# Performance work log

Hardware: AMD Instinct MI355X
Metric: run time of the kernel (lower is better)

Reference implementation:

```python
import jax, jax.numpy as jnp
import numpy as np

EMBED = 1024
HEADS = 16
HEAD_DIM = EMBED // HEADS


def setup_inputs() -> dict:
    key = jax.random.key(0)
    ks = jax.random.split(key, 9)
    s = 1.0 / np.sqrt(EMBED)
    inp = {
        "inputs": jax.random.normal(ks[0], (2, 2048, EMBED), dtype=jnp.float32),
        "Wq": jax.random.normal(ks[1], (EMBED, EMBED), dtype=jnp.float32) * s,
        "bq": jnp.zeros((EMBED,), dtype=jnp.float32),
        "Wk": jax.random.normal(ks[2], (EMBED, EMBED), dtype=jnp.float32) * s,
        "bk": jnp.zeros((EMBED,), dtype=jnp.float32),
        "Wv": jax.random.normal(ks[3], (EMBED, EMBED), dtype=jnp.float32) * s,
        "bv": jnp.zeros((EMBED,), dtype=jnp.float32),
        "Wo": jax.random.normal(ks[4], (EMBED, EMBED), dtype=jnp.float32) * s,
        "bo": jnp.zeros((EMBED,), dtype=jnp.float32),
    }
    return inp


def _split_heads(x, B, S):
    # [B, S, E] -> [B, H, S, D]
    return x.reshape(B, S, HEADS, HEAD_DIM).transpose(0, 2, 1, 3)


def reference(inputs, Wq, bq, Wk, bk, Wv, bv, Wo, bo):
    B, S, E = inputs.shape
    q = _split_heads(inputs @ Wq + bq, B, S)
    k = _split_heads(inputs @ Wk + bk, B, S)
    v = _split_heads(inputs @ Wv + bv, B, S)
    # scaled dot-product attention per the original: score scaled by sqrt(d_k)
    score = jnp.einsum("bhsd,bhtd->bhst", q, k) / jnp.sqrt(jnp.float32(HEAD_DIM))
    weights = jax.nn.softmax(score, axis=-1)
    attn = jnp.einsum("bhst,bhtd->bhsd", weights, v)
    concat = attn.transpose(0, 2, 1, 3).reshape(B, S, E)
    return concat @ Wo + bo
```

## Files before the change

kernel.cpp:

```cpp
#include <hip/hip_runtime.h>
#include <cmath>

#define EMBED 1024
#define HEADS 16
#define HDIM  64
#define BATCH 2
#define SEQ   2048
#define MTOT  (BATCH*SEQ)
#define KDIM  1024

typedef __attribute__((ext_vector_type(8))) short bf16x8;
typedef __attribute__((ext_vector_type(4))) float fx4;

#define MFMA(a,b,c) __builtin_amdgcn_mfma_f32_16x16x32_bf16((a),(b),(c),0,0,0)

__device__ __forceinline__ unsigned short f2bf(float x) {
    unsigned u = __float_as_uint(x);
    unsigned r = (u + 0x7FFFu + ((u >> 16) & 1u)) >> 16;
    return (unsigned short)r;
}
__device__ __forceinline__ float bf2f(unsigned short h) {
    return __uint_as_float(((unsigned)h) << 16);
}
__device__ __forceinline__ int swz_grp(int row, int grp) {
    return row * 64 + ((grp ^ (row & 7)) << 3);
}
__device__ __forceinline__ void gload16(const void* g, void* l) {
    __builtin_amdgcn_global_load_lds((const __attribute__((address_space(1))) void*)g,
                                     (__attribute__((address_space(3))) void*)l, 16, 0, 0);
}
__device__ __forceinline__ float dpp_qswap(float x) {
    return __int_as_float(__builtin_amdgcn_mov_dpp(__float_as_int(x), 0xB1, 0xF, 0xF, true));
}

#define C2S 0.18033688f

__global__ __launch_bounds__(256)
void prep(const float* __restrict__ X,
          const float* __restrict__ Wq, const float* __restrict__ Wk,
          const float* __restrict__ Wv, const float* __restrict__ Wo,
          unsigned short* __restrict__ Xh,
          unsigned short* __restrict__ WtH, unsigned short* __restrict__ WtL,
          unsigned short* __restrict__ WtOh, unsigned short* __restrict__ WtOl)
{
    const int bid = blockIdx.x;
    const int tid = threadIdx.x;
    if (bid < 2048) {
        int i = (bid * 256 + tid) * 8;
        float4 a = *(const float4*)(X + i);
        float4 b = *(const float4*)(X + i + 4);
        bf16x8 h;
        h[0] = (short)f2bf(a.x); h[1] = (short)f2bf(a.y);
        h[2] = (short)f2bf(a.z); h[3] = (short)f2bf(a.w);
        h[4] = (short)f2bf(b.x); h[5] = (short)f2bf(b.y);
        h[6] = (short)f2bf(b.z); h[7] = (short)f2bf(b.w);
        *(bf16x8*)(Xh + i) = h;
        return;
    }
    const int u = bid - 2048;
    const int z = u >> 8;
    const float* W = (z == 0) ? Wq : (z == 1) ? Wk : (z == 2) ? Wv : Wo;
    unsigned short* Th = (z < 3) ? WtH + (size_t)z * 1048576 : WtOh;
    unsigned short* Tl = (z == 2) ? WtL + (size_t)2 * 1048576 : WtOl;
    const bool wantLo = (z >= 2);
    const int k0 = ((u >> 4) & 15) * 64, n0 = (u & 15) * 64;

    __shared__ float t[64][65];
    #pragma unroll
    for (int it = 0; it < 4; ++it) {
        int v2 = tid + it * 256;
        int r = v2 >> 4, c4 = (v2 & 15) << 2;
        float4 v = *(const float4*)(W + (size_t)(k0 + r) * EMBED + n0 + c4);
        t[r][c4] = v.x; t[r][c4 + 1] = v.y; t[r][c4 + 2] = v.z; t[r][c4 + 3] = v.w;
    }
    __syncthreads();
    #pragma unroll
    for (int it = 0; it < 4; ++it) {
        int v2 = tid + it * 256;
        int r = v2 >> 4, c4 = (v2 & 15) << 2;
        ushort4 h, l;
        float x;
        x = t[c4 + 0][r]; h.x = f2bf(x); l.x = f2bf(x - bf2f(h.x));
        x = t[c4 + 1][r]; h.y = f2bf(x); l.y = f2bf(x - bf2f(h.y));
        x = t[c4 + 2][r]; h.z = f2bf(x); l.z = f2bf(x - bf2f(h.z));
        x = t[c4 + 3][r]; h.w = f2bf(x); l.w = f2bf(x - bf2f(h.w));
        *(ushort4*)(Th + (size_t)(n0 + r) * EMBED + k0 + c4) = h;
        if (wantLo)
            *(ushort4*)(Tl + (size_t)(n0 + r) * EMBED + k0 + c4) = l;
    }
}

__global__ __launch_bounds__(256, 2)
void gemm_qkv(const unsigned short* __restrict__ Xh,
              const unsigned short* __restrict__ WtH, const unsigned short* __restrict__ WtL,
              const float* __restrict__ bq, const float* __restrict__ bk,
              const float* __restrict__ bv,
              unsigned short* __restrict__ Qh, unsigned short* __restrict__ Khi,
              unsigned short* __restrict__ Vhi)
{
    __shared__ unsigned short Ah[8192];
    __shared__ unsigned short Bh[3][4096], Bl[4096];

    const int tid = threadIdx.x, lane = tid & 63, w = tid >> 6;
    const int wm = w >> 1, wn = w & 1;
    const int lin = (blockIdx.x & 7) * 64 + (blockIdx.x >> 3);
    const int m0 = (lin >> 4) * 128, n0 = (lin & 15) * 64;

    const char* aB = (const char*)(Xh + (size_t)m0 * KDIM);

    auto stageA = [&](int kt) {
        #pragma unroll
        for (int i = 0; i < 4; ++i) {
            int uw = (i << 12) + (w << 10);
            int u  = uw + (lane << 4);
            int row = u >> 7, grp = (u >> 4) & 7;
            size_t gb = (size_t)row * (KDIM * 2) + (size_t)kt * 128 + ((grp ^ (row & 7)) << 4);
            gload16(aB + gb, (char*)Ah + uw);
        }
    };
    auto stageB = [&](int kt, int which) {
        const char* bBh = (const char*)(WtH + (size_t)which * 1048576 + (size_t)n0 * KDIM);
        const char* bBl = (const char*)(WtL + (size_t)2 * 1048576 + (size_t)n0 * KDIM);
        #pragma unroll
        for (int i = 0; i < 2; ++i) {
            int uw = (i << 12) + (w << 10);
            int u  = uw + (lane << 4);
            int row = u >> 7, grp = (u >> 4) & 7;
            size_t gb = (size_t)row * (KDIM * 2) + (size_t)kt * 128 + ((grp ^ (row & 7)) << 4);
            gload16(bBh + gb, (char*)Bh[which] + uw);
            if (which == 2) gload16(bBl + gb, (char*)Bl + uw);
        }
    };

    const fx4 zero4 = {0.f, 0.f, 0.f, 0.f};
    fx4 acc[3][4][2];
    #pragma unroll
    for (int q = 0; q < 3; ++q)
        #pragma unroll
        for (int i = 0; i < 4; ++i) { acc[q][i][0] = zero4; acc[q][i][1] = zero4; }

    for (int kt = 0; kt < KDIM / 64; ++kt) {
        __syncthreads();
        stageA(kt);
        stageB(kt, 0);
        stageB(kt, 1);
        stageB(kt, 2);
        __syncthreads();
        #pragma unroll
        for (int kh = 0; kh < 2; ++kh) {
            const int grp = kh * 4 + (lane >> 4);
            bf16x8 ah[4];
            #pragma unroll
            for (int mi = 0; mi < 4; ++mi)
                ah[mi] = *(const bf16x8*)(Ah + swz_grp(wm * 64 + mi * 16 + (lane & 15), grp));
            #pragma unroll
            for (int q = 0; q < 2; ++q) {
                bf16x8 bh2[2];
                #pragma unroll
                for (int ni = 0; ni < 2; ++ni)
                    bh2[ni] = *(const bf16x8*)(Bh[q] + swz_grp(wn * 32 + ni * 16 + (lane & 15), grp));
                #pragma unroll
                for (int mi = 0; mi < 4; ++mi)
                    #pragma unroll
                    for (int ni = 0; ni < 2; ++ni)
                        acc[q][mi][ni] = MFMA(ah[mi], bh2[ni], acc[q][mi][ni]);
            }
            {
                bf16x8 bh2[2], bl2[2];
                #pragma unroll
                for (int ni = 0; ni < 2; ++ni) {
                    int off = swz_grp(wn * 32 + ni * 16 + (lane & 15), grp);
                    bh2[ni] = *(const bf16x8*)(Bh[2] + off);
                    bl2[ni] = *(const bf16x8*)(Bl + off);
                }
                #pragma unroll
                for (int mi = 0; mi < 4; ++mi)
                    #pragma unroll
                    for (int ni = 0; ni < 2; ++ni) {
                        acc[2][mi][ni] = MFMA(ah[mi], bh2[ni], acc[2][mi][ni]);
                        acc[2][mi][ni] = MFMA(ah[mi], bl2[ni], acc[2][mi][ni]);
                    }
            }
        }
    }

    const int hh = n0 >> 6;
    #pragma unroll
    for (int q = 0; q < 3; ++q) {
        const float* bias = (q == 0) ? bq : (q == 1) ? bk : bv;
        #pragma unroll
        for (int mi = 0; mi < 4; ++mi)
            #pragma unroll
            for (int ni = 0; ni < 2; ++ni) {
                const int n = n0 + wn * 32 + ni * 16 + (lane & 15);
                const float bb = bias[n];
                const int d = n & 63;
                if (q < 2) {
                    unsigned short* plane = (q == 0) ? Qh : Khi;
                    #pragma unroll
                    for (int reg = 0; reg < 4; ++reg) {
                        const int m = m0 + wm * 64 + mi * 16 + (lane >> 4) * 4 + reg;
                        const int b = m >> 11, s = m & (SEQ - 1);
                        float val = acc[q][mi][ni][reg] + bb;
                        if (q == 0) val *= C2S;
                        plane[((size_t)(b * HEADS + hh) * SEQ + s) * HDIM + d] = f2bf(val);
                    }
                } else {
                    const int m = m0 + wm * 64 + mi * 16 + (lane >> 4) * 4;
                    const int b = m >> 11, s = m & (SEQ - 1);
                    const int sl = s & 63;
                    const int c = (sl & 32) | ((sl & 12) << 1) | ((sl & 16) >> 2);
                    ushort4 o;
                    o.x = f2bf(acc[2][mi][ni][0] + bb);
                    o.y = f2bf(acc[2][mi][ni][1] + bb);
                    o.z = f2bf(acc[2][mi][ni][2] + bb);
                    o.w = f2bf(acc[2][mi][ni][3] + bb);
                    *(ushort4*)(Vhi + ((size_t)(b * HEADS + hh) * HDIM + d) * SEQ
                                + (s & ~63) + c) = o;
                }
            }
    }
}

__global__ __launch_bounds__(256, 2)
void gemm_ao(const unsigned short* __restrict__ AOh,
             const unsigned short* __restrict__ Bgh, const unsigned short* __restrict__ Bgl,
             const float* __restrict__ bias, float* __restrict__ Cf)
{
    __shared__ unsigned short Ah[8192];
    __shared__ unsigned short Bh[4096], Bl[4096];

    const int tid = threadIdx.x, lane = tid & 63, w = tid >> 6;
    const int wm = w >> 1, wn = w & 1;
    const int lin = (blockIdx.x & 7) * 64 + (blockIdx.x >> 3);
    const int m0 = (lin >> 4) * 128, n0 = (lin & 15) * 64;

    const char* aB  = (const char*)(AOh + (size_t)m0 * KDIM);
    const char* bBh = (const char*)(Bgh + (size_t)n0 * KDIM);
    const char* bBl = (const char*)(Bgl + (size_t)n0 * KDIM);

    auto stageA = [&](int kt) {
        #pragma unroll
        for (int i = 0; i < 4; ++i) {
            int uw = (i << 12) + (w << 10);
            int u  = uw + (lane << 4);
            int row = u >> 7, grp = (u >> 4) & 7;
            size_t gb = (size_t)row * (KDIM * 2) + (size_t)kt * 128 + ((grp ^ (row & 7)) << 4);
            gload16(aB + gb, (char*)Ah + uw);
        }
    };
    auto stageB = [&](int kt) {
        #pragma unroll
        for (int i = 0; i < 2; ++i) {
            int uw = (i << 12) + (w << 10);
            int u  = uw + (lane << 4);
            int row = u >> 7, grp = (u >> 4) & 7;
            size_t gb = (size_t)row * (KDIM * 2) + (size_t)kt * 128 + ((grp ^ (row & 7)) << 4);
            gload16(bBh + gb, (char*)Bh + uw);
            gload16(bBl + gb, (char*)Bl + uw);
        }
    };

    const fx4 zero4 = {0.f, 0.f, 0.f, 0.f};
    fx4 acc[4][2];
    #pragma unroll
    for (int i = 0; i < 4; ++i) { acc[i][0] = zero4; acc[i][1] = zero4; }

    for (int kt = 0; kt < KDIM / 64; ++kt) {
        __syncthreads();
        stageA(kt);
        stageB(kt);
        __syncthreads();
        #pragma unroll
        for (int kh = 0; kh < 2; ++kh) {
            const int grp = kh * 4 + (lane >> 4);
            bf16x8 ah[4], bh2[2], bl2[2];
            #pragma unroll
            for (int mi = 0; mi < 4; ++mi)
                ah[mi] = *(const bf16x8*)(Ah + swz_grp(wm * 64 + mi * 16 + (lane & 15), grp));
            #pragma unroll
            for (int ni = 0; ni < 2; ++ni) {
                int off = swz_grp(wn * 32 + ni * 16 + (lane & 15), grp);
                bh2[ni] = *(const bf16x8*)(Bh + off);
                bl2[ni] = *(const bf16x8*)(Bl + off);
            }
            #pragma unroll
            for (int mi = 0; mi < 4; ++mi)
                #pragma unroll
                for (int ni = 0; ni < 2; ++ni) {
                    acc[mi][ni] = MFMA(ah[mi], bh2[ni], acc[mi][ni]);
                    acc[mi][ni] = MFMA(ah[mi], bl2[ni], acc[mi][ni]);
                }
        }
    }

    #pragma unroll
    for (int mi = 0; mi < 4; ++mi)
        #pragma unroll
        for (int ni = 0; ni < 2; ++ni) {
            const int n = n0 + wn * 32 + ni * 16 + (lane & 15);
            const float bb = bias[n];
            #pragma unroll
            for (int reg = 0; reg < 4; ++reg) {
                const int m = m0 + wm * 64 + mi * 16 + (lane >> 4) * 4 + reg;
                Cf[(size_t)m * EMBED + n] = acc[mi][ni][reg] + bb;
            }
        }
}

__global__ __launch_bounds__(256, 4)
void attn_mfma(const unsigned short* __restrict__ Qh,
               const unsigned short* __restrict__ Khi,
               const unsigned short* __restrict__ Vhi, unsigned short* __restrict__ AOh)
{
    __shared__ unsigned short Ks[2][4096];
    __shared__ unsigned short Vs[2][4096];

    const int tid = threadIdx.x, lane = tid & 63, w = tid >> 6;
    const int xcd = blockIdx.x & 7, loc = blockIdx.x >> 3;
    const int bh = xcd * 4 + (loc >> 5);
    const int q0 = (loc & 31) * 64;
    const size_t qkBase = (size_t)bh * SEQ * HDIM;

    auto stageKV = [&](int kv0, int buf) {
        const char* baseK = (const char*)(Khi + qkBase + (size_t)kv0 * HDIM);
        const char* baseV = (const char*)(Vhi + (size_t)bh * HDIM * SEQ + kv0);
        #pragma unroll
        for (int i = 0; i < 2; ++i) {
            int uw = (i << 12) + (w << 10);
            int u  = uw + (lane << 4);
            int row = u >> 7, grp = (u >> 4) & 7;
            size_t gk = (size_t)row * 128 + ((grp ^ (row & 7)) << 4);
            size_t gv = (size_t)row * (SEQ * 2) + ((grp ^ (row & 7)) << 4);
            gload16(baseK + gk, (char*)Ks[buf] + uw);
            gload16(baseV + gv, (char*)Vs[buf] + uw);
        }
    };

    bf16x8 qf[2];
    #pragma unroll
    for (int kh = 0; kh < 2; ++kh) {
        const int row = q0 + w * 16 + (lane & 15);
        const int grp = kh * 4 + (lane >> 4);
        qf[kh] = *(const bf16x8*)(Qh + qkBase + (size_t)row * HDIM + grp * 8);
    }

    const fx4 zero4 = {0.f, 0.f, 0.f, 0.f};
    fx4 acco[4];
    fx4 accl = zero4;
    #pragma unroll
    for (int df = 0; df < 4; ++df) acco[df] = zero4;

    bf16x8 ones;
    #pragma unroll
    for (int i = 0; i < 8; ++i) ones[i] = (short)0x3F80;

    stageKV(0, 0);
    __syncthreads();

    for (int t = 0; t < 32; ++t) {
        const int cur = t & 1;
        if (t < 31) stageKV((t + 1) * 64, cur ^ 1);

        fx4 s4[4] = {zero4, zero4, zero4, zero4};
        __builtin_amdgcn_s_setprio(1);
        #pragma unroll
        for (int kh = 0; kh < 2; ++kh) {
            const int grp = kh * 4 + (lane >> 4);
            bf16x8 kf[4];
            #pragma unroll
            for (int nf = 0; nf < 4; ++nf)
                kf[nf] = *(const bf16x8*)(Ks[cur] + swz_grp(nf * 16 + (lane & 15), grp));
            #pragma unroll
            for (int nf = 0; nf < 4; ++nf)
                s4[nf] = MFMA(kf[nf], qf[kh], s4[nf]);
        }
        __builtin_amdgcn_s_setprio(0);

        float p[4][4];
        #pragma unroll
        for (int kvf = 0; kvf < 4; ++kvf)
            #pragma unroll
            for (int reg = 0; reg < 4; ++reg) {
                float e;
                asm("v_exp_f32 %0, %1\n\ts_nop 0" : "=v"(e) : "v"(s4[kvf][reg]));
                p[kvf][reg] = e;
            }

        bf16x8 pa[2];
        #pragma unroll
        for (int t2 = 0; t2 < 2; ++t2) {
            union { unsigned u[4]; bf16x8 v; } pk;
            asm("v_cvt_pk_bf16_f32 %0, %1, %2" : "=v"(pk.u[0])
                : "v"(p[2 * t2][0]), "v"(p[2 * t2][1]));
            asm("v_cvt_pk_bf16_f32 %0, %1, %2" : "=v"(pk.u[1])
                : "v"(p[2 * t2][2]), "v"(p[2 * t2][3]));
            asm("v_cvt_pk_bf16_f32 %0, %1, %2" : "=v"(pk.u[2])
                : "v"(p[2 * t2 + 1][0]), "v"(p[2 * t2 + 1][1]));
            asm("v_cvt_pk_bf16_f32 %0, %1, %2" : "=v"(pk.u[3])
                : "v"(p[2 * t2 + 1][2]), "v"(p[2 * t2 + 1][3]));
            pa[t2] = pk.v;
        }

        __builtin_amdgcn_s_setprio(1);
        #pragma unroll
        for (int t2 = 0; t2 < 2; ++t2) {
            const int grp = t2 * 4 + (lane >> 4);
            accl = MFMA(pa[t2], ones, accl);
            #pragma unroll
            for (int df = 0; df < 4; ++df) {
                bf16x8 vh = *(const bf16x8*)(Vs[cur] + swz_grp(df * 16 + (lane & 15), grp));
                acco[df] = MFMA(pa[t2], vh, acco[df]);
            }
        }
        __builtin_amdgcn_s_setprio(0);

        __syncthreads();
    }

    const int b = bh >> 4, h = bh & 15;
    const int parity = lane & 1;
    float inv[4];
    #pragma unroll
    for (int reg = 0; reg < 4; ++reg) inv[reg] = __builtin_amdgcn_rcpf(accl[reg]);
    #pragma unroll
    for (int df = 0; df < 4; ++df) {
        const int d0 = df * 16 + ((lane & 15) & ~1);
        #pragma unroll
        for (int rp = 0; rp < 4; rp += 2) {
            float ve = acco[df][rp]     * inv[rp];
            float vo = acco[df][rp + 1] * inv[rp + 1];
            float e_sw = dpp_qswap(ve), o_sw = dpp_qswap(vo);
            float a  = parity ? o_sw : ve;
            float b2 = parity ? vo   : e_sw;
            unsigned u;
            asm volatile("v_cvt_pk_bf16_f32 %0, %1, %2" : "=v"(u) : "v"(a), "v"(b2));
            const int q = q0 + w * 16 + (lane >> 4) * 4 + rp + parity;
            *(unsigned int*)(AOh + ((size_t)(b * SEQ + q) * EMBED + h * HDIM + d0)) = u;
        }
    }
}

extern "C" void kernel_launch(void* const* d_in, const int* in_sizes, int n_in,
                              void* d_out, int out_size, void* d_ws, size_t ws_size,
                              hipStream_t stream)
{
    (void)in_sizes; (void)n_in; (void)out_size; (void)ws_size;

    const float* X  = (const float*)d_in[0];
    const float* Wq = (const float*)d_in[1];
    const float* bq = (const float*)d_in[2];
    const float* Wk = (const float*)d_in[3];
    const float* bk = (const float*)d_in[4];
    const float* Wv = (const float*)d_in[5];
    const float* bv = (const float*)d_in[6];
    const float* Wo = (const float*)d_in[7];
    const float* bo = (const float*)d_in[8];

    const size_t R_us = (size_t)8 * 1024 * 1024;
    unsigned short* us = (unsigned short*)d_ws;
    unsigned short* Qh   = us + 0 * R_us;
    unsigned short* WtOh = us + 0 * R_us + 4194304;
    unsigned short* WtOl = us + 0 * R_us + 5242880;
    unsigned short* Khi  = us + 1 * R_us;
    unsigned short* Vhi  = us + 2 * R_us;
    unsigned short* AOh  = us + 3 * R_us;
    unsigned short* WtH  = us + 3 * R_us;
    unsigned short* WtL  = WtH + (size_t)3 * 1048576;
    unsigned short* Xh   = (unsigned short*)d_out;

    const dim3 blk(256);

    prep<<<dim3(3072), blk, 0, stream>>>(X, Wq, Wk, Wv, Wo, Xh, WtH, WtL, WtOh, WtOl);

    gemm_qkv<<<dim3(512), blk, 0, stream>>>(Xh, WtH, WtL, bq, bk, bv, Qh, Khi, Vhi);

    attn_mfma<<<dim3(1024), blk, 0, stream>>>(Qh, Khi, Vhi, AOh);

    gemm_ao<<<dim3(512), blk, 0, stream>>>(AOh, WtOh, WtOl, bo, (float*)d_out);
}
```

Before: 112.6 us.

## Drop bf16 split-precision low weights and split QKV GEMM across grid y

Removes the hi/lo bf16 split of the Wv and Wo weights, so the V projection and output GEMM each do one MFMA per tile instead of two, and prep no longer writes the low-part planes. The fused QKV GEMM is split into three launches along blockIdx.y, one per projection, with a smaller accumulator set and less shared memory. Occupancy hints rise from 2 to 4 blocks per CU. The trade is lower accuracy in V and the output projection, which the split had been added to protect, and the A tile is now loaded three times.

```diff
diff --git a/kernel.cpp b/kernel.cpp
--- a/kernel.cpp
+++ b/kernel.cpp
@@ -40,8 +40,7 @@
           const float* __restrict__ Wq, const float* __restrict__ Wk,
           const float* __restrict__ Wv, const float* __restrict__ Wo,
           unsigned short* __restrict__ Xh,
-          unsigned short* __restrict__ WtH, unsigned short* __restrict__ WtL,
-          unsigned short* __restrict__ WtOh, unsigned short* __restrict__ WtOl)
+          unsigned short* __restrict__ WtH, unsigned short* __restrict__ WtOh)
 {
     const int bid = blockIdx.x;
     const int tid = threadIdx.x;
@@ -61,8 +60,6 @@
     const int z = u >> 8;
     const float* W = (z == 0) ? Wq : (z == 1) ? Wk : (z == 2) ? Wv : Wo;
     unsigned short* Th = (z < 3) ? WtH + (size_t)z * 1048576 : WtOh;
-    unsigned short* Tl = (z == 2) ? WtL + (size_t)2 * 1048576 : WtOl;
-    const bool wantLo = (z >= 2);
     const int k0 = ((u >> 4) & 15) * 64, n0 = (u & 15) * 64;
 
     __shared__ float t[64][65];
@@ -78,35 +75,34 @@
     for (int it = 0; it < 4; ++it) {
         int v2 = tid + it * 256;
         int r = v2 >> 4, c4 = (v2 & 15) << 2;
-        ushort4 h, l;
-        float x;
-        x = t[c4 + 0][r]; h.x = f2bf(x); l.x = f2bf(x - bf2f(h.x));
-        x = t[c4 + 1][r]; h.y = f2bf(x); l.y = f2bf(x - bf2f(h.y));
-        x = t[c4 + 2][r]; h.z = f2bf(x); l.z = f2bf(x - bf2f(h.z));
-        x = t[c4 + 3][r]; h.w = f2bf(x); l.w = f2bf(x - bf2f(h.w));
+        ushort4 h;
+        h.x = f2bf(t[c4 + 0][r]);
+        h.y = f2bf(t[c4 + 1][r]);
+        h.z = f2bf(t[c4 + 2][r]);
+        h.w = f2bf(t[c4 + 3][r]);
         *(ushort4*)(Th + (size_t)(n0 + r) * EMBED + k0 + c4) = h;
-        if (wantLo)
-            *(ushort4*)(Tl + (size_t)(n0 + r) * EMBED + k0 + c4) = l;
-    }
-}
-
-__global__ __launch_bounds__(256, 2)
+    }
+}
+
+__global__ __launch_bounds__(256, 4)
 void gemm_qkv(const unsigned short* __restrict__ Xh,
-              const unsigned short* __restrict__ WtH, const unsigned short* __restrict__ WtL,
+              const unsigned short* __restrict__ WtH,
               const float* __restrict__ bq, const float* __restrict__ bk,
               const float* __restrict__ bv,
               unsigned short* __restrict__ Qh, unsigned short* __restrict__ Khi,
               unsigned short* __restrict__ Vhi)
 {
     __shared__ unsigned short Ah[8192];
-    __shared__ unsigned short Bh[3][4096], Bl[4096];
+    __shared__ unsigned short Bh[4096];
 
     const int tid = threadIdx.x, lane = tid & 63, w = tid >> 6;
     const int wm = w >> 1, wn = w & 1;
+    const int which = blockIdx.y;
     const int lin = (blockIdx.x & 7) * 64 + (blockIdx.x >> 3);
     const int m0 = (lin >> 4) * 128, n0 = (lin & 15) * 64;
 
-    const char* aB = (const char*)(Xh + (size_t)m0 * KDIM);
+    const char* aB  = (const char*)(Xh + (size_t)m0 * KDIM);
+    const char* bB  = (const char*)(WtH + (size_t)which * 1048576 + (size_t)n0 * KDIM);
 
     auto stageA = [&](int kt) {
         #pragma unroll
@@ -118,126 +114,95 @@
             gload16(aB + gb, (char*)Ah + uw);
         }
     };
-    auto stageB = [&](int kt, int which) {
-        const char* bBh = (const char*)(WtH + (size_t)which * 1048576 + (size_t)n0 * KDIM);
-        const char* bBl = (const char*)(WtL + (size_t)2 * 1048576 + (size_t)n0 * KDIM);
+    auto stageB = [&](int kt) {
         #pragma unroll
         for (int i = 0; i < 2; ++i) {
             int uw = (i << 12) + (w << 10);
             int u  = uw + (lane << 4);
             int row = u >> 7, grp = (u >> 4) & 7;
             size_t gb = (size_t)row * (KDIM * 2) + (size_t)kt * 128 + ((grp ^ (row & 7)) << 4);
-            gload16(bBh + gb, (char*)Bh[which] + uw);
-            if (which == 2) gload16(bBl + gb, (char*)Bl + uw);
+            gload16(bB + gb, (char*)Bh + uw);
         }
     };
 
     const fx4 zero4 = {0.f, 0.f, 0.f, 0.f};
-    fx4 acc[3][4][2];
-    #pragma unroll
-    for (int q = 0; q < 3; ++q)
-        #pragma unroll
-        for (int i = 0; i < 4; ++i) { acc[q][i][0] = zero4; acc[q][i][1] = zero4; }
+    fx4 acc[4][2];
+    #pragma unroll
+    for (int i = 0; i < 4; ++i) { acc[i][0] = zero4; acc[i][1] = zero4; }
 
     for (int kt = 0; kt < KDIM / 64; ++kt) {
         __syncthreads();
         stageA(kt);
-        stageB(kt, 0);
-        stageB(kt, 1);
-        stageB(kt, 2);
+        stageB(kt);
         __syncthreads();
         #pragma unroll
         for (int kh = 0; kh < 2; ++kh) {
             const int grp = kh * 4 + (lane >> 4);
-            bf16x8 ah[4];
+            bf16x8 ah[4], bh2[2];
             #pragma unroll
             for (int mi = 0; mi < 4; ++mi)
                 ah[mi] = *(const bf16x8*)(Ah + swz_grp(wm * 64 + mi * 16 + (lane & 15), grp));
             #pragma unroll
-            for (int q = 0; q < 2; ++q) {
-                bf16x8 bh2[2];
+            for (int ni = 0; ni < 2; ++ni)
+                bh2[ni] = *(const bf16x8*)(Bh + swz_grp(wn * 32 + ni * 16 + (lane & 15), grp));
+            #pragma unroll
+            for (int mi = 0; mi < 4; ++mi)
                 #pragma unroll
                 for (int ni = 0; ni < 2; ++ni)
-                    bh2[ni] = *(const bf16x8*)(Bh[q] + swz_grp(wn * 32 + ni * 16 + (lane & 15), grp));
+                    acc[mi][ni] = MFMA(ah[mi], bh2[ni], acc[mi][ni]);
+        }
+    }
+
+    const int hh = n0 >> 6;
+    const float* bias = (which == 0) ? bq : (which == 1) ? bk : bv;
+    #pragma unroll
+    for (int mi = 0; mi < 4; ++mi)
+        #pragma unroll
+        for (int ni = 0; ni < 2; ++ni) {
+            const int n = n0 + wn * 32 + ni * 16 + (lane & 15);
+            const float bb = bias[n];
+            const int d = n & 63;
+            if (which < 2) {
+                unsigned short* plane = (which == 0) ? Qh : Khi;
                 #pragma unroll
-                for (int mi = 0; mi < 4; ++mi)
-                    #pragma unroll
-                    for (int ni = 0; ni < 2; ++ni)
-                        acc[q][mi][ni] = MFMA(ah[mi], bh2[ni], acc[q][mi][ni]);
+                for (int reg = 0; reg < 4; ++reg) {
+                    const int m = m0 + wm * 64 + mi * 16 + (lane >> 4) * 4 + reg;
+                    const int b = m >> 11, s = m & (SEQ - 1);
+                    float val = acc[mi][ni][reg] + bb;
+                    if (which == 0) val *= C2S;
+                    plane[((size_t)(b * HEADS + hh) * SEQ + s) * HDIM + d] = f2bf(val);
+                }
+            } else {
+                const int m = m0 + wm * 64 + mi * 16 + (lane >> 4) * 4;
+                const int b = m >> 11, s = m & (SEQ - 1);
+                const int sl = s & 63;
+                const int c = (sl & 32) | ((sl & 12) << 1) | ((sl & 16) >> 2);
+                ushort4 o;
+                o.x = f2bf(acc[mi][ni][0] + bb);
+                o.y = f2bf(acc[mi][ni][1] + bb);
+                o.z = f2bf(acc[mi][ni][2] + bb);
+                o.w = f2bf(acc[mi][ni][3] + bb);
+                *(ushort4*)(Vhi + ((size_t)(b * HEADS + hh) * HDIM + d) * SEQ
+                            + (s & ~63) + c) = o;
             }
-            {
-                bf16x8 bh2[2], bl2[2];
-                #pragma unroll
-                for (int ni = 0; ni < 2; ++ni) {
-                    int off = swz_grp(wn * 32 + ni * 16 + (lane & 15), grp);
-                    bh2[ni] = *(const bf16x8*)(Bh[2] + off);
-                    bl2[ni] = *(const bf16x8*)(Bl + off);
-                }
-                #pragma unroll
-                for (int mi = 0; mi < 4; ++mi)
-                    #pragma unroll
-                    for (int ni = 0; ni < 2; ++ni) {
-                        acc[2][mi][ni] = MFMA(ah[mi], bh2[ni], acc[2][mi][ni]);
-                        acc[2][mi][ni] = MFMA(ah[mi], bl2[ni], acc[2][mi][ni]);
-                    }
-            }
-        }
-    }
-
-    const int hh = n0 >> 6;
-    #pragma unroll
-    for (int q = 0; q < 3; ++q) {
-        const float* bias = (q == 0) ? bq : (q == 1) ? bk : bv;
-        #pragma unroll
-        for (int mi = 0; mi < 4; ++mi)
-            #pragma unroll
-            for (int ni = 0; ni < 2; ++ni) {
-                const int n = n0 + wn * 32 + ni * 16 + (lane & 15);
-                const float bb = bias[n];
-                const int d = n & 63;
-                if (q < 2) {
-                    unsigned short* plane = (q == 0) ? Qh : Khi;
-                    #pragma unroll
-                    for (int reg = 0; reg < 4; ++reg) {
-                        const int m = m0 + wm * 64 + mi * 16 + (lane >> 4) * 4 + reg;
-                        const int b = m >> 11, s = m & (SEQ - 1);
-                        float val = acc[q][mi][ni][reg] + bb;
-                        if (q == 0) val *= C2S;
-                        plane[((size_t)(b * HEADS + hh) * SEQ + s) * HDIM + d] = f2bf(val);
-                    }
-                } else {
-                    const int m = m0 + wm * 64 + mi * 16 + (lane >> 4) * 4;
-                    const int b = m >> 11, s = m & (SEQ - 1);
-                    const int sl = s & 63;
-                    const int c = (sl & 32) | ((sl & 12) << 1) | ((sl & 16) >> 2);
-                    ushort4 o;
-                    o.x = f2bf(acc[2][mi][ni][0] + bb);
-                    o.y = f2bf(acc[2][mi][ni][1] + bb);
-                    o.z = f2bf(acc[2][mi][ni][2] + bb);
-                    o.w = f2bf(acc[2][mi][ni][3] + bb);
-                    *(ushort4*)(Vhi + ((size_t)(b * HEADS + hh) * HDIM + d) * SEQ
-                                + (s & ~63) + c) = o;
-                }
-            }
-    }
-}
-
-__global__ __launch_bounds__(256, 2)
+        }
+}
+
+__global__ __launch_bounds__(256, 4)
 void gemm_ao(const unsigned short* __restrict__ AOh,
-             const unsigned short* __restrict__ Bgh, const unsigned short* __restrict__ Bgl,
+             const unsigned short* __restrict__ Bgh,
              const float* __restrict__ bias, float* __restrict__ Cf)
 {
     __shared__ unsigned short Ah[8192];
-    __shared__ unsigned short Bh[4096], Bl[4096];
+    __shared__ unsigned short Bh[4096];
 
     const int tid = threadIdx.x, lane = tid & 63, w = tid >> 6;
     const int wm = w >> 1, wn = w & 1;
     const int lin = (blockIdx.x & 7) * 64 + (blockIdx.x >> 3);
     const int m0 = (lin >> 4) * 128, n0 = (lin & 15) * 64;
 
-    const char* aB  = (const char*)(AOh + (size_t)m0 * KDIM);
-    const char* bBh = (const char*)(Bgh + (size_t)n0 * KDIM);
-    const char* bBl = (const char*)(Bgl + (size_t)n0 * KDIM);
+    const char* aB = (const char*)(AOh + (size_t)m0 * KDIM);
+    const char* bB = (const char*)(Bgh + (size_t)n0 * KDIM);
 
     auto stageA = [&](int kt) {
         #pragma unroll
@@ -256,8 +221,7 @@
             int u  = uw + (lane << 4);
             int row = u >> 7, grp = (u >> 4) & 7;
             size_t gb = (size_t)row * (KDIM * 2) + (size_t)kt * 128 + ((grp ^ (row & 7)) << 4);
-            gload16(bBh + gb, (char*)Bh + uw);
-            gload16(bBl + gb, (char*)Bl + uw);
+            gload16(bB + gb, (char*)Bh + uw);
         }
     };
 
@@ -274,23 +238,18 @@
         #pragma unroll
         for (int kh = 0; kh < 2; ++kh) {
             const int grp = kh * 4 + (lane >> 4);
-            bf16x8 ah[4], bh2[2], bl2[2];
+            bf16x8 ah[4], bh2[2];
             #pragma unroll
             for (int mi = 0; mi < 4; ++mi)
                 ah[mi] = *(const bf16x8*)(Ah + swz_grp(wm * 64 + mi * 16 + (lane & 15), grp));
             #pragma unroll
-            for (int ni = 0; ni < 2; ++ni) {
-                int off = swz_grp(wn * 32 + ni * 16 + (lane & 15), grp);
-                bh2[ni] = *(const bf16x8*)(Bh + off);
-                bl2[ni] = *(const bf16x8*)(Bl + off);
-            }
+            for (int ni = 0; ni < 2; ++ni)
+                bh2[ni] = *(const bf16x8*)(Bh + swz_grp(wn * 32 + ni * 16 + (lane & 15), grp));
             #pragma unroll
             for (int mi = 0; mi < 4; ++mi)
                 #pragma unroll
-                for (int ni = 0; ni < 2; ++ni) {
+                for (int ni = 0; ni < 2; ++ni)
                     acc[mi][ni] = MFMA(ah[mi], bh2[ni], acc[mi][ni]);
-                    acc[mi][ni] = MFMA(ah[mi], bl2[ni], acc[mi][ni]);
-                }
         }
     }
 
@@ -461,21 +420,19 @@
     unsigned short* us = (unsigned short*)d_ws;
     unsigned short* Qh   = us + 0 * R_us;
     unsigned short* WtOh = us + 0 * R_us + 4194304;
-    unsigned short* WtOl = us + 0 * R_us + 5242880;
     unsigned short* Khi  = us + 1 * R_us;
     unsigned short* Vhi  = us + 2 * R_us;
     unsigned short* AOh  = us + 3 * R_us;
     unsigned short* WtH  = us + 3 * R_us;
-    unsigned short* WtL  = WtH + (size_t)3 * 1048576;
     unsigned short* Xh   = (unsigned short*)d_out;
 
     const dim3 blk(256);
 
-    prep<<<dim3(3072), blk, 0, stream>>>(X, Wq, Wk, Wv, Wo, Xh, WtH, WtL, WtOh, WtOl);
-
-    gemm_qkv<<<dim3(512), blk, 0, stream>>>(Xh, WtH, WtL, bq, bk, bv, Qh, Khi, Vhi);
+    prep<<<dim3(3072), blk, 0, stream>>>(X, Wq, Wk, Wv, Wo, Xh, WtH, WtOh);
+
+    gemm_qkv<<<dim3(512, 3), blk, 0, stream>>>(Xh, WtH, bq, bk, bv, Qh, Khi, Vhi);
 
     attn_mfma<<<dim3(1024), blk, 0, stream>>>(Qh, Khi, Vhi, AOh);
 
-    gemm_ao<<<dim3(512), blk, 0, stream>>>(AOh, WtOh, WtOl, bo, (float*)d_out);
-}
+    gemm_ao<<<dim3(512), blk, 0, stream>>>(AOh, WtOh, bo, (float*)d_out);
+}
```

Result: faster. 110.3 us (-2.1%).
